# Kernel tuning notes

Measured on AMD Instinct MI355X. Metric: run time of the kernel, lower is better.

The kernel has to match this reference:

```python
import jax, jax.numpy as jnp
import numpy as np

WS = 8      # window_size
NH = 8      # n_heads
EPS = 1e-06


def _rel_coords(ws):
    # Swin-style relative position index table, matches torch buffer construction
    c = np.stack(np.meshgrid(np.arange(ws), np.arange(ws), indexing='ij'))  # [2,ws,ws]
    c = c.reshape(2, -1)                      # [2, L]
    rel = c[:, :, None] - c[:, None, :]       # [2, L, L]
    rel = rel.transpose(1, 2, 0) + (ws - 1)   # [L, L, 2]
    rel[:, :, 0] *= 2 * ws - 1
    return jnp.asarray(rel.sum(-1), dtype=jnp.int32)  # [L, L]


def rms_film(x, t, gw, bw):
    # x: [B,C,H,W], t: [B,d_t]; RMS over channel dim, FiLM scale/shift from t
    g = (t @ gw.T)[:, :, None, None]
    b = (t @ bw.T)[:, :, None, None]
    return g * x * jax.lax.rsqrt(jnp.mean(x * x, axis=1, keepdims=True) + EPS) + b


def window_attn(x, wq, wk, wv, wo_w, wo_b, rpb):
    B, C, H, W = x.shape
    h, w = H // WS, W // WS
    L = WS * WS
    dh = C // NH
    # partition into windows: [B, h, w, L, C]
    xw = x.reshape(B, C, h, WS, w, WS).transpose(0, 2, 4, 3, 5, 1).reshape(B, h, w, L, C)

    def heads(p):
        y = xw @ p.T  # Linear, no bias
        return y.reshape(B, h, w, L, NH, dh).transpose(0, 1, 2, 4, 3, 5)  # [B,h,w,n,L,dh]

    q, k, v = heads(wq), heads(wk), heads(wv)
    bias = rpb[:, _rel_coords(WS)]  # [NH, L, L] gather from bias table
    attn = jnp.einsum('bhwnld,bhwnmd->bhwnlm', q, k) / float(np.sqrt(dh)) + bias
    o = jnp.einsum('bhwnlm,bhwnmd->bhwnld', jax.nn.softmax(attn, axis=-1), v)
    # merge windows, channel order (n c): [B, NH*dh, H, W]
    o = o.reshape(B, h, w, NH, WS, WS, dh).transpose(0, 3, 6, 1, 4, 2, 5).reshape(B, C, H, W)
    # 1x1 conv output projection (with bias)
    return jnp.einsum('bchw,oc->bohw', o, wo_w) + wo_b[None, :, None, None]


def convnext(x, t, dw_w, dw_b, gw, bw, w1, b1, w2, b2):
    # 7x7 depthwise conv, pad 3
    y = jax.lax.conv_general_dilated(
        x, dw_w, window_strides=(1, 1), padding=[(3, 3), (3, 3)],
        dimension_numbers=('NCHW', 'OIHW', 'NCHW'), feature_group_count=x.shape[1])
    y = y + dw_b[None, :, None, None]
    y = rms_film(y, t, gw, bw).transpose(0, 2, 3, 1)  # -> NHWC
    y = jax.nn.gelu(y @ w1.T + b1, approximate=False) @ w2.T + b2
    return y.transpose(0, 3, 1, 2)


def setup_inputs() -> dict:
    key = jax.random.key(0)
    ks = jax.random.split(key, 16)
    D, DT, B, H, W = 256, 256, 8, 128, 128
    DH = 4 * D
    n = lambda k, s: jax.random.normal(k, s, jnp.float32) * 0.02
    return dict(
        x=jax.random.normal(ks[0], (B, D, H, W), jnp.float32),
        t=jax.random.normal(ks[1], (B, DT), jnp.float32),
        an_g=n(ks[2], (D, DT)), an_b=n(ks[3], (D, DT)),
        wq=n(ks[4], (D, D)), wk=n(ks[5], (D, D)), wv=n(ks[6], (D, D)),
        wo_w=n(ks[7], (D, D)), wo_b=jnp.zeros((D,), jnp.float32),
        rpb=n(ks[8], (NH, (2 * WS - 1) ** 2)),
        dw_w=n(ks[9], (D, 1, 7, 7)), dw_b=jnp.zeros((D,), jnp.float32),
        fn_g=n(ks[10], (D, DT)), fn_b=n(ks[11], (D, DT)),
        w1=n(ks[12], (DH, D)), b1=jnp.zeros((DH,), jnp.float32),
        w2=n(ks[13], (D, DH)), b2=jnp.zeros((D,), jnp.float32))


def reference(x, t, an_g, an_b, wq, wk, wv, wo_w, wo_b, rpb,
              dw_w, dw_b, fn_g, fn_b, w1, b1, w2, b2):
    x = x + window_attn(rms_film(x, t, an_g, an_b), wq, wk, wv, wo_w, wo_b, rpb)
    return x + convnext(x, t, dw_w, dw_b, fn_g, fn_b, w1, b1, w2, b2)
```

## Files before the change

kernel.cpp:

```cpp
#include <hip/hip_runtime.h>
#include <math.h>

typedef __attribute__((ext_vector_type(8))) short bf16x8_t;
typedef __attribute__((ext_vector_type(4))) float f32x4;

__device__ __forceinline__ unsigned short f2bf(float f) {
  unsigned int u = __builtin_bit_cast(unsigned int, f);
  u += 0x7FFFu + ((u >> 16) & 1u);
  return (unsigned short)(u >> 16);
}
__device__ __forceinline__ float bf2f(unsigned short h) {
  unsigned int u = ((unsigned int)h) << 16;
  return __builtin_bit_cast(float, u);
}

typedef const __attribute__((address_space(1))) void* as1cv;
typedef __attribute__((address_space(3))) void* as3v;

__device__ __forceinline__ void gld_lds16(const unsigned short* g, unsigned short* l) {
  __builtin_amdgcn_global_load_lds((as1cv)g, (as3v)l, 16, 0, 0);
}

__global__ __launch_bounds__(256) void tvec_kernel(const float* __restrict__ t,
    const float* __restrict__ an_g, const float* __restrict__ an_b,
    const float* __restrict__ fn_g, const float* __restrict__ fn_b,
    float* __restrict__ gvec) {
  int d = threadIdx.x;
  int b = blockIdx.x;
  int m = blockIdx.y;
  __shared__ float ts[256];
  ts[d] = t[b * 256 + d];
  __syncthreads();
  const float* W = (m == 0) ? an_g : (m == 1) ? an_b : (m == 2) ? fn_g : fn_b;
  float acc = 0.f;
  #pragma unroll 8
  for (int k = 0; k < 256; ++k) acc += ts[k] * W[d * 256 + k];
  gvec[(m * 8 + b) * 256 + d] = acc;
}

__global__ __launch_bounds__(256) void wconv_kernel(const float* __restrict__ wq,
    const float* __restrict__ wk, const float* __restrict__ wv, const float* __restrict__ wo,
    const float* __restrict__ w1, const float* __restrict__ w2,
    unsigned short* __restrict__ outp) {
  int i = blockIdx.x * 256 + threadIdx.x;
  const float* src; int off;
  if      (i <  65536) { src = wq; off = 0; }
  else if (i < 131072) { src = wk; off = 65536; }
  else if (i < 196608) { src = wv; off = 131072; }
  else if (i < 262144) { src = wo; off = 196608; }
  else if (i < 524288) { src = w1; off = 262144; }
  else                 { src = w2; off = 524288; }
  outp[i] = f2bf(src[i - off]);
}

template<int IS_BF>
__global__ __launch_bounds__(256) void film_kernel(const void* __restrict__ in_,
    const float* __restrict__ gvec, int gsel, unsigned short* __restrict__ outbf) {
  const float* inf = (const float*)in_;
  const unsigned short* inb = (const unsigned short*)in_;
  int blk = blockIdx.x;
  int b = blk >> 8;
  int p0 = (blk & 255) << 6;
  int lane = threadIdx.x & 63;
  int cg = threadIdx.x >> 6;
  __shared__ unsigned short vals[64][264];
  __shared__ float ssred[4][64];
  __shared__ float rinvs[64];
  size_t base = ((size_t)b << 22) + p0;
  float ss = 0.f;
  #pragma unroll 4
  for (int ci = 0; ci < 64; ++ci) {
    int c = (cg << 6) + ci;
    size_t idx = base + ((size_t)c << 14) + lane;
    float v = IS_BF ? bf2f(inb[idx]) : inf[idx];
    ss += v * v;
    vals[lane][c] = f2bf(v);
  }
  ssred[cg][lane] = ss;
  __syncthreads();
  if (threadIdx.x < 64) {
    float s = ssred[0][threadIdx.x] + ssred[1][threadIdx.x] + ssred[2][threadIdx.x] + ssred[3][threadIdx.x];
    rinvs[threadIdx.x] = rsqrtf(s * (1.0f / 256.0f) + 1e-6f);
  }
  __syncthreads();
  int pix = threadIdx.x >> 2;
  int c0 = (threadIdx.x & 3) << 6;
  float rv = rinvs[pix];
  const float* gp = gvec + ((gsel * 2 + 0) * 8 + b) * 256;
  const float* bp = gvec + ((gsel * 2 + 1) * 8 + b) * 256;
  unsigned short* orow = outbf + (((size_t)b << 14) + p0 + pix) * 256 + c0;
  #pragma unroll
  for (int ch = 0; ch < 8; ++ch) {
    bf16x8_t pack;
    #pragma unroll
    for (int e = 0; e < 8; ++e) {
      int c = c0 + ch * 8 + e;
      float v = bf2f(vals[pix][c]);
      float o = gp[c] * v * rv + bp[c];
      pack[e] = (short)f2bf(o);
    }
    *(bf16x8_t*)(orow + ch * 8) = pack;
  }
}

template<int DO_GELU>
__global__ __launch_bounds__(256) void gemm_kernel(const unsigned short* __restrict__ A,
    const unsigned short* __restrict__ Bw, const float* __restrict__ bias,
    unsigned short* __restrict__ outp, int K, int N) {
  __shared__ unsigned short As[128 * 64];
  __shared__ unsigned short Bs[128 * 64];
  int tid = threadIdx.x;
  int m0 = blockIdx.x << 7;
  int n0 = blockIdx.y << 7;
  int w = tid >> 6, lane = tid & 63;
  int wm = (w >> 1) << 6, wn = (w & 1) << 6;
  f32x4 acc[4][4];
  #pragma unroll
  for (int mi = 0; mi < 4; ++mi)
    #pragma unroll
    for (int ni = 0; ni < 4; ++ni)
      acc[mi][ni] = (f32x4){0.f, 0.f, 0.f, 0.f};

  for (int k0 = 0; k0 < K; k0 += 64) {
    #pragma unroll
    for (int r2 = 0; r2 < 4; ++r2) {
      int linear = (r2 << 8) + tid;
      int row = linear >> 3;
      int ch = linear & 7;
      gld_lds16(A  + (size_t)(m0 + row) * K + k0 + ch * 8, As + linear * 8);
      gld_lds16(Bw + (size_t)(n0 + row) * K + k0 + ch * 8, Bs + linear * 8);
    }
    __syncthreads();
    #pragma unroll
    for (int kk = 0; kk < 64; kk += 32) {
      bf16x8_t af[4], bq[4];
      int lr = lane & 15;
      int lk = ((lane >> 4) << 3) + kk;
      #pragma unroll
      for (int mi = 0; mi < 4; ++mi)
        af[mi] = *(const bf16x8_t*)(As + ((wm + (mi << 4) + lr) << 6) + lk);
      #pragma unroll
      for (int ni = 0; ni < 4; ++ni)
        bq[ni] = *(const bf16x8_t*)(Bs + ((wn + (ni << 4) + lr) << 6) + lk);
      #pragma unroll
      for (int mi = 0; mi < 4; ++mi)
        #pragma unroll
        for (int ni = 0; ni < 4; ++ni)
          acc[mi][ni] = __builtin_amdgcn_mfma_f32_16x16x32_bf16(af[mi], bq[ni], acc[mi][ni], 0, 0, 0);
    }
    __syncthreads();
  }
  int lr = lane & 15, lg = lane >> 4;
  #pragma unroll
  for (int mi = 0; mi < 4; ++mi) {
    #pragma unroll
    for (int ni = 0; ni < 4; ++ni) {
      int col = n0 + wn + (ni << 4) + lr;
      int row = m0 + wm + (mi << 4) + (lg << 2);
      f32x4 a = acc[mi][ni];
      #pragma unroll
      for (int i = 0; i < 4; ++i) {
        float v = a[i];
        if (DO_GELU) {
          v += bias[col];
          v = 0.5f * v * (1.0f + erff(v * 0.70710678118654752f));
        }
        outp[(size_t)(row + i) * N + col] = f2bf(v);
      }
    }
  }
}

__global__ __launch_bounds__(256) void gemm_t_kernel(const unsigned short* __restrict__ A,
    const unsigned short* __restrict__ Bw, unsigned short* __restrict__ outp) {
  __shared__ unsigned short smem[16384];
  unsigned short* As = smem;
  unsigned short* Bs = smem + 8192;
  const int K = 256;
  int tid = threadIdx.x;
  int m0 = blockIdx.x << 7;
  int n0 = blockIdx.y << 7;
  int w = tid >> 6, lane = tid & 63;
  int wm = (w >> 1) << 6, wn = (w & 1) << 6;
  f32x4 acc[4][4];
  #pragma unroll
  for (int mi = 0; mi < 4; ++mi)
    #pragma unroll
    for (int ni = 0; ni < 4; ++ni)
      acc[mi][ni] = (f32x4){0.f, 0.f, 0.f, 0.f};

  for (int k0 = 0; k0 < K; k0 += 64) {
    #pragma unroll
    for (int r2 = 0; r2 < 4; ++r2) {
      int linear = (r2 << 8) + tid;
      int row = linear >> 3;
      int ch = linear & 7;
      gld_lds16(A  + (size_t)(m0 + row) * K + k0 + ch * 8, As + linear * 8);
      gld_lds16(Bw + (size_t)(n0 + row) * K + k0 + ch * 8, Bs + linear * 8);
    }
    __syncthreads();
    #pragma unroll
    for (int kk = 0; kk < 64; kk += 32) {
      bf16x8_t af[4], bq[4];
      int lr = lane & 15;
      int lk = ((lane >> 4) << 3) + kk;
      #pragma unroll
      for (int mi = 0; mi < 4; ++mi)
        af[mi] = *(const bf16x8_t*)(As + ((wm + (mi << 4) + lr) << 6) + lk);
      #pragma unroll
      for (int ni = 0; ni < 4; ++ni)
        bq[ni] = *(const bf16x8_t*)(Bs + ((wn + (ni << 4) + lr) << 6) + lk);
      #pragma unroll
      for (int mi = 0; mi < 4; ++mi)
        #pragma unroll
        for (int ni = 0; ni < 4; ++ni)
          acc[mi][ni] = __builtin_amdgcn_mfma_f32_16x16x32_bf16(af[mi], bq[ni], acc[mi][ni], 0, 0, 0);
    }
    __syncthreads();
  }

  int lr = lane & 15, lg = lane >> 4;
  #pragma unroll
  for (int mi = 0; mi < 4; ++mi)
    #pragma unroll
    for (int ni = 0; ni < 4; ++ni) {
      int cl = wn + (ni << 4) + lr;
      int rl = wm + (mi << 4) + (lg << 2);
      f32x4 a = acc[mi][ni];
      #pragma unroll
      for (int i = 0; i < 4; ++i)
        smem[cl * 128 + rl + i] = f2bf(a[i]);
    }
  __syncthreads();

  int cl = tid >> 1;
  int half = tid & 1;
  int b = m0 >> 14;
  int pix = (m0 & 16383) + half * 64;
  int c = n0 + cl;
  const unsigned short* srow = smem + cl * 128 + half * 64;
  unsigned short* orow = outp + ((size_t)b * 256 + c) * 16384 + pix;
  #pragma unroll
  for (int jj = 0; jj < 8; ++jj)
    *(bf16x8_t*)(orow + jj * 8) = *(const bf16x8_t*)(srow + jj * 8);
}

__global__ __launch_bounds__(256) void gemm2f_kernel(const unsigned short* __restrict__ A,
    const unsigned short* __restrict__ Bw, const float* __restrict__ bias,
    const unsigned short* __restrict__ x1, float* __restrict__ outp, int m_base) {
  __shared__ unsigned short smem[16384];
  unsigned short* As = smem;
  unsigned short* Bs = smem + 8192;
  const int K = 1024, N = 256;
  int tid = threadIdx.x;
  int m0 = blockIdx.x << 7;
  int n0 = blockIdx.y << 7;
  int w = tid >> 6, lane = tid & 63;
  int wm = (w >> 1) << 6, wn = (w & 1) << 6;
  f32x4 acc[4][4];
  #pragma unroll
  for (int mi = 0; mi < 4; ++mi)
    #pragma unroll
    for (int ni = 0; ni < 4; ++ni)
      acc[mi][ni] = (f32x4){0.f, 0.f, 0.f, 0.f};

  for (int k0 = 0; k0 < K; k0 += 64) {
    #pragma unroll
    for (int r2 = 0; r2 < 4; ++r2) {
      int linear = (r2 << 8) + tid;
      int row = linear >> 3;
      int ch = linear & 7;
      gld_lds16(A  + (size_t)(m0 + row) * K + k0 + ch * 8, As + linear * 8);
      gld_lds16(Bw + (size_t)(n0 + row) * K + k0 + ch * 8, Bs + linear * 8);
    }
    __syncthreads();
    #pragma unroll
    for (int kk = 0; kk < 64; kk += 32) {
      bf16x8_t af[4], bq[4];
      int lr = lane & 15;
      int lk = ((lane >> 4) << 3) + kk;
      #pragma unroll
      for (int mi = 0; mi < 4; ++mi)
        af[mi] = *(const bf16x8_t*)(As + ((wm + (mi << 4) + lr) << 6) + lk);
      #pragma unroll
      for (int ni = 0; ni < 4; ++ni)
        bq[ni] = *(const bf16x8_t*)(Bs + ((wn + (ni << 4) + lr) << 6) + lk);
      #pragma unroll
      for (int mi = 0; mi < 4; ++mi)
        #pragma unroll
        for (int ni = 0; ni < 4; ++ni)
          acc[mi][ni] = __builtin_amdgcn_mfma_f32_16x16x32_bf16(af[mi], bq[ni], acc[mi][ni], 0, 0, 0);
    }
    __syncthreads();
  }

  int lr = lane & 15, lg = lane >> 4;
  #pragma unroll
  for (int mi = 0; mi < 4; ++mi)
    #pragma unroll
    for (int ni = 0; ni < 4; ++ni) {
      int cl = wn + (ni << 4) + lr;
      int rl = wm + (mi << 4) + (lg << 2);
      f32x4 a = acc[mi][ni];
      #pragma unroll
      for (int i = 0; i < 4; ++i)
        smem[cl * 128 + rl + i] = f2bf(a[i]);
    }
  __syncthreads();

  int cl = tid >> 1;
  int half = tid & 1;
  int pglob0 = m_base + m0;
  int b = pglob0 >> 14;
  int pix = (pglob0 & 16383) + half * 64;
  int c = n0 + cl;
  const unsigned short* srow = smem + cl * 128 + half * 64;
  size_t gbase = ((size_t)b * 256 + c) * 16384 + pix;
  const unsigned short* xrow = x1 + gbase;
  float* orow = outp + gbase;
  float bb = bias[c];
  #pragma unroll
  for (int jj = 0; jj < 8; ++jj) {
    bf16x8_t sv = *(const bf16x8_t*)(srow + jj * 8);
    bf16x8_t xv = *(const bf16x8_t*)(xrow + jj * 8);
    #pragma unroll
    for (int e = 0; e < 8; ++e)
      orow[jj * 8 + e] = bf2f((unsigned short)sv[e]) + bf2f((unsigned short)xv[e]) + bb;
  }
}

__global__ __launch_bounds__(256, 3) void attn_kernel(const unsigned short* __restrict__ qg,
    const unsigned short* __restrict__ kg, const unsigned short* __restrict__ vt,
    const float* __restrict__ rpb, unsigned short* __restrict__ og) {
  __shared__ float rpbf[1800];
  __shared__ unsigned short pbuf[4][64 * 72];
  int wi = blockIdx.x;
  int b = wi >> 8, wh = (wi >> 4) & 15, ww = wi & 15;
  int tid = threadIdx.x;
  int w = tid >> 6, lane = tid & 63;
  int g = lane >> 4, lr = lane & 15;
  for (int idx = tid; idx < 1800; idx += 256) rpbf[idx] = rpb[idx];
  __syncthreads();

  int rowpix = (wh * 8) * 128 + ww * 8;
  size_t ibase = ((size_t)b << 14) + rowpix;
  unsigned short* pb = pbuf[w];
  const float scale = 0.17677669529663689f;

  #pragma unroll 1
  for (int hh = 0; hh < 2; ++hh) {
    int h = w * 2 + hh;
    float sums[4][4];
    {
      bf16x8_t qf[4], kf[4];
      #pragma unroll
      for (int t = 0; t < 4; ++t) {
        size_t tok = ibase + (size_t)(t * 2 + (lr >> 3)) * 128 + (lr & 7);
        qf[t] = *(const bf16x8_t*)(qg + tok * 256 + h * 32 + g * 8);
        kf[t] = *(const bf16x8_t*)(kg + tok * 256 + h * 32 + g * 8);
      }
      f32x4 sacc[4][4];
      #pragma unroll
      for (int qt = 0; qt < 4; ++qt)
        #pragma unroll
        for (int kt = 0; kt < 4; ++kt)
          sacc[qt][kt] = __builtin_amdgcn_mfma_f32_16x16x32_bf16(qf[qt], kf[kt],
                           (f32x4){0.f, 0.f, 0.f, 0.f}, 0, 0, 0);
      const float* rb = &rpbf[h * 225];
      #pragma unroll
      for (int qt = 0; qt < 4; ++qt) {
        #pragma unroll
        for (int i = 0; i < 4; ++i) {
          int q = qt * 16 + g * 4 + i;
          int il = q >> 3, jl = q & 7;
          float v[4];
          #pragma unroll
          for (int kt = 0; kt < 4; ++kt) {
            int kv = kt * 16 + lr;
            v[kt] = sacc[qt][kt][i] * scale + rb[(il - (kv >> 3) + 7) * 15 + (jl - (kv & 7) + 7)];
          }
          float mx = fmaxf(fmaxf(v[0], v[1]), fmaxf(v[2], v[3]));
          mx = fmaxf(mx, __shfl_xor(mx, 1));
          mx = fmaxf(mx, __shfl_xor(mx, 2));
          mx = fmaxf(mx, __shfl_xor(mx, 4));
          mx = fmaxf(mx, __shfl_xor(mx, 8));
          float sm = 0.f;
          #pragma unroll
          for (int kt = 0; kt < 4; ++kt) { v[kt] = __expf(v[kt] - mx); sm += v[kt]; }
          sm += __shfl_xor(sm, 1);
          sm += __shfl_xor(sm, 2);
          sm += __shfl_xor(sm, 4);
          sm += __shfl_xor(sm, 8);
          sums[qt][i] = sm;
          #pragma unroll
          for (int kt = 0; kt < 4; ++kt)
            pb[q * 72 + kt * 16 + lr] = f2bf(v[kt]);
        }
      }
    }
    f32x4 oacc[4][2];
    #pragma unroll
    for (int qt = 0; qt < 4; ++qt) {
      oacc[qt][0] = (f32x4){0.f, 0.f, 0.f, 0.f};
      oacc[qt][1] = (f32x4){0.f, 0.f, 0.f, 0.f};
    }
    #pragma unroll
    for (int ks = 0; ks < 2; ++ks) {
      bf16x8_t pf[4], vf[2];
      #pragma unroll
      for (int qt = 0; qt < 4; ++qt)
        pf[qt] = *(const bf16x8_t*)(pb + (qt * 16 + lr) * 72 + ks * 32 + g * 8);
      #pragma unroll
      for (int dt = 0; dt < 2; ++dt) {
        size_t plane = (size_t)b * 256 + h * 32 + dt * 16 + lr;
        vf[dt] = *(const bf16x8_t*)(vt + (plane << 14) + rowpix + (size_t)(ks * 4 + g) * 128);
      }
      #pragma unroll
      for (int qt = 0; qt < 4; ++qt)
        #pragma unroll
        for (int dt = 0; dt < 2; ++dt)
          oacc[qt][dt] = __builtin_amdgcn_mfma_f32_16x16x32_bf16(pf[qt], vf[dt], oacc[qt][dt], 0, 0, 0);
    }
    #pragma unroll
    for (int qt = 0; qt < 4; ++qt) {
      #pragma unroll
      for (int i = 0; i < 4; ++i) {
        int q = qt * 16 + g * 4 + i;
        float inv = 1.0f / sums[qt][i];
        size_t tok = ibase + (size_t)(q >> 3) * 128 + (q & 7);
        #pragma unroll
        for (int dt = 0; dt < 2; ++dt)
          og[tok * 256 + h * 32 + dt * 16 + lr] = f2bf(oacc[qt][dt][i] * inv);
      }
    }
  }
}

__global__ __launch_bounds__(256) void addt1_kernel(const unsigned short* __restrict__ src,
    const float* __restrict__ resid, const float* __restrict__ bias,
    unsigned short* __restrict__ outp) {
  int blk = blockIdx.x;
  int b = blk >> 8;
  int p0 = (blk & 255) << 6;
  __shared__ unsigned short vals[64][264];
  int tid = threadIdx.x;
  #pragma unroll
  for (int r = 0; r < 8; ++r) {
    int linear = r * 256 + tid;
    int row = linear >> 5;
    int ch = linear & 31;
    bf16x8_t v = *(const bf16x8_t*)(src + (((size_t)b << 14) + p0 + row) * 256 + ch * 8);
    *(bf16x8_t*)(&vals[row][ch * 8]) = v;
  }
  __syncthreads();
  int lane = tid & 63;
  int cq = tid >> 6;
  #pragma unroll 4
  for (int ci = 0; ci < 64; ++ci) {
    int c = (cq << 6) + ci;
    float v = bf2f(vals[lane][c]);
    size_t gidx = ((size_t)b << 22) + ((size_t)c << 14) + p0 + lane;
    outp[gidx] = f2bf(resid[gidx] + v + bias[c]);
  }
}

__global__ __launch_bounds__(256) void dwconv_kernel(const unsigned short* __restrict__ x1,
    const float* __restrict__ w, const float* __restrict__ bias, unsigned short* __restrict__ outp) {
  int bc = blockIdx.y;
  int c = bc & 255;
  int y0 = blockIdx.x << 6;
  __shared__ unsigned short tile[70 * 144];
  __shared__ float wf[49];
  const unsigned short* plane = x1 + ((size_t)bc << 14);
  int tid = threadIdx.x;

  for (int idx = tid; idx < 70 * 16; idx += 256) {
    int row = idx >> 4, ch = idx & 15;
    int gy = y0 - 3 + row;
    bf16x8_t v = (bf16x8_t){0, 0, 0, 0, 0, 0, 0, 0};
    if (gy >= 0 && gy < 128) v = *(const bf16x8_t*)(plane + gy * 128 + ch * 8);
    *(bf16x8_t*)(&tile[row * 144 + 8 + ch * 8]) = v;
  }
  for (int idx = tid; idx < 70 * 6; idx += 256) {
    int row = idx / 6, e = idx % 6;
    int col = (e < 3) ? (5 + e) : (133 + e);
    tile[row * 144 + col] = 0;
  }
  if (tid < 49) wf[tid] = w[c * 49 + tid];
  __syncthreads();

  int r = tid >> 2;
  int c0 = (tid & 3) << 5;
  float acc[32];
  float bb = bias[c];
  #pragma unroll
  for (int i = 0; i < 32; ++i) acc[i] = bb;

  #pragma unroll
  for (int u = 0; u < 7; ++u) {
    const unsigned short* rowp = &tile[(r + u) * 144 + c0];
    float f[48];
    #pragma unroll
    for (int k = 0; k < 6; ++k) {
      bf16x8_t v = *(const bf16x8_t*)(rowp + k * 8);
      #pragma unroll
      for (int e = 0; e < 8; ++e) f[k * 8 + e] = bf2f((unsigned short)v[e]);
    }
    #pragma unroll
    for (int t = 0; t < 7; ++t) {
      float wv = wf[u * 7 + t];
      #pragma unroll
      for (int i = 0; i < 32; ++i) acc[i] += f[i + 5 + t] * wv;
    }
  }

  unsigned short* orow = outp + ((size_t)bc << 14) + (size_t)(y0 + r) * 128 + c0;
  #pragma unroll
  for (int k = 0; k < 4; ++k) {
    bf16x8_t v;
    #pragma unroll
    for (int e = 0; e < 8; ++e) v[e] = (short)f2bf(acc[k * 8 + e]);
    *(bf16x8_t*)(orow + k * 8) = v;
  }
}

extern "C" void kernel_launch(void* const* d_in, const int* in_sizes, int n_in,
                              void* d_out, int out_size, void* d_ws, size_t ws_size,
                              hipStream_t stream) {
  const float* x    = (const float*)d_in[0];
  const float* t    = (const float*)d_in[1];
  const float* an_g = (const float*)d_in[2];
  const float* an_b = (const float*)d_in[3];
  const float* wq   = (const float*)d_in[4];
  const float* wk   = (const float*)d_in[5];
  const float* wv   = (const float*)d_in[6];
  const float* wo_w = (const float*)d_in[7];
  const float* wo_b = (const float*)d_in[8];
  const float* rpb  = (const float*)d_in[9];
  const float* dw_w = (const float*)d_in[10];
  const float* dw_b = (const float*)d_in[11];
  const float* fn_g = (const float*)d_in[12];
  const float* fn_b = (const float*)d_in[13];
  const float* w1   = (const float*)d_in[14];
  const float* b1   = (const float*)d_in[15];
  const float* w2   = (const float*)d_in[16];
  const float* b2   = (const float*)d_in[17];
  float* outp = (float*)d_out;

  char* ws = (char*)d_ws;
  const size_t MB = 1024ull * 1024ull;
  float* gvec = (float*)ws;
  unsigned short* wbf = (unsigned short*)(ws + 32768);
  unsigned short* P = (unsigned short*)(ws + 2 * MB);
  unsigned short* Q = (unsigned short*)(ws + 66 * MB);
  unsigned short* R = (unsigned short*)(ws + 130 * MB);
  unsigned short* vbuf = (unsigned short*)((char*)d_out + 64 * MB);

  unsigned short* wq_bf = wbf;
  unsigned short* wk_bf = wbf + 65536;
  unsigned short* wv_bf = wbf + 131072;
  unsigned short* wo_bf = wbf + 196608;
  unsigned short* w1_bf = wbf + 262144;
  unsigned short* w2_bf = wbf + 524288;

  tvec_kernel<<<dim3(8, 4), 256, 0, stream>>>(t, an_g, an_b, fn_g, fn_b, gvec);
  wconv_kernel<<<3072, 256, 0, stream>>>(wq, wk, wv, wo_w, w1, w2, wbf);

  film_kernel<0><<<2048, 256, 0, stream>>>(x, gvec, 0, P);

  gemm_kernel<0><<<dim3(1024, 2), 256, 0, stream>>>(P, wq_bf, nullptr, Q, 256, 256);
  gemm_kernel<0><<<dim3(1024, 2), 256, 0, stream>>>(P, wk_bf, nullptr, R, 256, 256);
  gemm_t_kernel<<<dim3(1024, 2), 256, 0, stream>>>(P, wv_bf, vbuf);

  attn_kernel<<<2048, 256, 0, stream>>>(Q, R, vbuf, rpb, P);

  gemm_kernel<0><<<dim3(1024, 2), 256, 0, stream>>>(P, wo_bf, nullptr, Q, 256, 256);
  addt1_kernel<<<2048, 256, 0, stream>>>(Q, x, wo_b, R);

  dwconv_kernel<<<dim3(2, 2048), 256, 0, stream>>>(R, dw_w, dw_b, Q);
  film_kernel<1><<<2048, 256, 0, stream>>>(Q, gvec, 1, P);

  for (int qtr = 0; qtr < 4; ++qtr) {
    int m_base = qtr * 32768;
    gemm_kernel<1><<<dim3(256, 8), 256, 0, stream>>>(P + (size_t)m_base * 256, w1_bf, b1, Q, 256, 1024);
    gemm2f_kernel<<<dim3(256, 2), 256, 0, stream>>>(Q, w2_bf, b2, R, outp, m_base);
  }
}
```

Baseline: 958.1 us.

## Fuse output projection with residual add and store bf16 copy of input

The first FiLM pass now also writes a bf16 copy of x into the output buffer. The standalone residual-add/transposition kernel is removed, and a new GEMM epilogue adds bias and the bf16 residual while writing channel-major output directly. This cuts one full kernel's memory round trip at the cost of an extra bf16 write in film and lower residual precision (bf16 x instead of fp32). The attention kernel's block-to-window mapping is also permuted, interleaving batches across consecutive blocks.

```diff
diff --git a/kernel.cpp b/kernel.cpp
--- a/kernel.cpp
+++ b/kernel.cpp
@@ -53,9 +53,10 @@
   outp[i] = f2bf(src[i - off]);
 }
 
-template<int IS_BF>
+template<int IS_BF, int WX>
 __global__ __launch_bounds__(256) void film_kernel(const void* __restrict__ in_,
-    const float* __restrict__ gvec, int gsel, unsigned short* __restrict__ outbf) {
+    const float* __restrict__ gvec, int gsel, unsigned short* __restrict__ outbf,
+    unsigned short* __restrict__ xbf) {
   const float* inf = (const float*)in_;
   const unsigned short* inb = (const unsigned short*)in_;
   int blk = blockIdx.x;
@@ -74,7 +75,9 @@
     size_t idx = base + ((size_t)c << 14) + lane;
     float v = IS_BF ? bf2f(inb[idx]) : inf[idx];
     ss += v * v;
-    vals[lane][c] = f2bf(v);
+    unsigned short hv = f2bf(v);
+    vals[lane][c] = hv;
+    if (WX) xbf[idx] = hv;
   }
   ssred[cg][lane] = ss;
   __syncthreads();
@@ -243,6 +246,91 @@
   #pragma unroll
   for (int jj = 0; jj < 8; ++jj)
     *(bf16x8_t*)(orow + jj * 8) = *(const bf16x8_t*)(srow + jj * 8);
+}
+
+__global__ __launch_bounds__(256) void gemm_wof_kernel(const unsigned short* __restrict__ A,
+    const unsigned short* __restrict__ Bw, const float* __restrict__ bias,
+    const unsigned short* __restrict__ xbf, unsigned short* __restrict__ outp) {
+  __shared__ unsigned short smem[16384];
+  unsigned short* As = smem;
+  unsigned short* Bs = smem + 8192;
+  const int K = 256;
+  int tid = threadIdx.x;
+  int m0 = blockIdx.x << 7;
+  int n0 = blockIdx.y << 7;
+  int w = tid >> 6, lane = tid & 63;
+  int wm = (w >> 1) << 6, wn = (w & 1) << 6;
+  f32x4 acc[4][4];
+  #pragma unroll
+  for (int mi = 0; mi < 4; ++mi)
+    #pragma unroll
+    for (int ni = 0; ni < 4; ++ni)
+      acc[mi][ni] = (f32x4){0.f, 0.f, 0.f, 0.f};
+
+  for (int k0 = 0; k0 < K; k0 += 64) {
+    #pragma unroll
+    for (int r2 = 0; r2 < 4; ++r2) {
+      int linear = (r2 << 8) + tid;
+      int row = linear >> 3;
+      int ch = linear & 7;
+      gld_lds16(A  + (size_t)(m0 + row) * K + k0 + ch * 8, As + linear * 8);
+      gld_lds16(Bw + (size_t)(n0 + row) * K + k0 + ch * 8, Bs + linear * 8);
+    }
+    __syncthreads();
+    #pragma unroll
+    for (int kk = 0; kk < 64; kk += 32) {
+      bf16x8_t af[4], bq[4];
+      int lr = lane & 15;
+      int lk = ((lane >> 4) << 3) + kk;
+      #pragma unroll
+      for (int mi = 0; mi < 4; ++mi)
+        af[mi] = *(const bf16x8_t*)(As + ((wm + (mi << 4) + lr) << 6) + lk);
+      #pragma unroll
+      for (int ni = 0; ni < 4; ++ni)
+        bq[ni] = *(const bf16x8_t*)(Bs + ((wn + (ni << 4) + lr) << 6) + lk);
+      #pragma unroll
+      for (int mi = 0; mi < 4; ++mi)
+        #pragma unroll
+        for (int ni = 0; ni < 4; ++ni)
+          acc[mi][ni] = __builtin_amdgcn_mfma_f32_16x16x32_bf16(af[mi], bq[ni], acc[mi][ni], 0, 0, 0);
+    }
+    __syncthreads();
+  }
+
+  int lr = lane & 15, lg = lane >> 4;
+  #pragma unroll
+  for (int mi = 0; mi < 4; ++mi)
+    #pragma unroll
+    for (int ni = 0; ni < 4; ++ni) {
+      int cl = wn + (ni << 4) + lr;
+      int rl = wm + (mi << 4) + (lg << 2);
+      f32x4 a = acc[mi][ni];
+      #pragma unroll
+      for (int i = 0; i < 4; ++i)
+        smem[cl * 128 + rl + i] = f2bf(a[i]);
+    }
+  __syncthreads();
+
+  int cl = tid >> 1;
+  int half = tid & 1;
+  int b = m0 >> 14;
+  int pix = (m0 & 16383) + half * 64;
+  int c = n0 + cl;
+  const unsigned short* srow = smem + cl * 128 + half * 64;
+  size_t gbase = ((size_t)b * 256 + c) * 16384 + pix;
+  const unsigned short* xrow = xbf + gbase;
+  unsigned short* orow = outp + gbase;
+  float bb = bias[c];
+  #pragma unroll
+  for (int jj = 0; jj < 8; ++jj) {
+    bf16x8_t sv = *(const bf16x8_t*)(srow + jj * 8);
+    bf16x8_t xv = *(const bf16x8_t*)(xrow + jj * 8);
+    bf16x8_t ov;
+    #pragma unroll
+    for (int e = 0; e < 8; ++e)
+      ov[e] = (short)f2bf(bf2f((unsigned short)sv[e]) + bf2f((unsigned short)xv[e]) + bb);
+    *(bf16x8_t*)(orow + jj * 8) = ov;
+  }
 }
 
 __global__ __launch_bounds__(256) void gemm2f_kernel(const unsigned short* __restrict__ A,
@@ -334,7 +422,7 @@
     const float* __restrict__ rpb, unsigned short* __restrict__ og) {
   __shared__ float rpbf[1800];
   __shared__ unsigned short pbuf[4][64 * 72];
-  int wi = blockIdx.x;
+  int wi = (blockIdx.x & 7) * 256 + (blockIdx.x >> 3);
   int b = wi >> 8, wh = (wi >> 4) & 15, ww = wi & 15;
   int tid = threadIdx.x;
   int w = tid >> 6, lane = tid & 63;
@@ -436,34 +524,6 @@
   }
 }
 
-__global__ __launch_bounds__(256) void addt1_kernel(const unsigned short* __restrict__ src,
-    const float* __restrict__ resid, const float* __restrict__ bias,
-    unsigned short* __restrict__ outp) {
-  int blk = blockIdx.x;
-  int b = blk >> 8;
-  int p0 = (blk & 255) << 6;
-  __shared__ unsigned short vals[64][264];
-  int tid = threadIdx.x;
-  #pragma unroll
-  for (int r = 0; r < 8; ++r) {
-    int linear = r * 256 + tid;
-    int row = linear >> 5;
-    int ch = linear & 31;
-    bf16x8_t v = *(const bf16x8_t*)(src + (((size_t)b << 14) + p0 + row) * 256 + ch * 8);
-    *(bf16x8_t*)(&vals[row][ch * 8]) = v;
-  }
-  __syncthreads();
-  int lane = tid & 63;
-  int cq = tid >> 6;
-  #pragma unroll 4
-  for (int ci = 0; ci < 64; ++ci) {
-    int c = (cq << 6) + ci;
-    float v = bf2f(vals[lane][c]);
-    size_t gidx = ((size_t)b << 22) + ((size_t)c << 14) + p0 + lane;
-    outp[gidx] = f2bf(resid[gidx] + v + bias[c]);
-  }
-}
-
 __global__ __launch_bounds__(256) void dwconv_kernel(const unsigned short* __restrict__ x1,
     const float* __restrict__ w, const float* __restrict__ bias, unsigned short* __restrict__ outp) {
   int bc = blockIdx.y;
@@ -554,6 +614,7 @@
   unsigned short* P = (unsigned short*)(ws + 2 * MB);
   unsigned short* Q = (unsigned short*)(ws + 66 * MB);
   unsigned short* R = (unsigned short*)(ws + 130 * MB);
+  unsigned short* xbf  = (unsigned short*)d_out;
   unsigned short* vbuf = (unsigned short*)((char*)d_out + 64 * MB);
 
   unsigned short* wq_bf = wbf;
@@ -566,7 +627,7 @@
   tvec_kernel<<<dim3(8, 4), 256, 0, stream>>>(t, an_g, an_b, fn_g, fn_b, gvec);
   wconv_kernel<<<3072, 256, 0, stream>>>(wq, wk, wv, wo_w, w1, w2, wbf);
 
-  film_kernel<0><<<2048, 256, 0, stream>>>(x, gvec, 0, P);
+  film_kernel<0, 1><<<2048, 256, 0, stream>>>(x, gvec, 0, P, xbf);
 
   gemm_kernel<0><<<dim3(1024, 2), 256, 0, stream>>>(P, wq_bf, nullptr, Q, 256, 256);
   gemm_kernel<0><<<dim3(1024, 2), 256, 0, stream>>>(P, wk_bf, nullptr, R, 256, 256);
@@ -574,11 +635,10 @@
 
   attn_kernel<<<2048, 256, 0, stream>>>(Q, R, vbuf, rpb, P);
 
-  gemm_kernel<0><<<dim3(1024, 2), 256, 0, stream>>>(P, wo_bf, nullptr, Q, 256, 256);
-  addt1_kernel<<<2048, 256, 0, stream>>>(Q, x, wo_b, R);
+  gemm_wof_kernel<<<dim3(1024, 2), 256, 0, stream>>>(P, wo_bf, wo_b, xbf, R);
 
   dwconv_kernel<<<dim3(2, 2048), 256, 0, stream>>>(R, dw_w, dw_b, Q);
-  film_kernel<1><<<2048, 256, 0, stream>>>(Q, gvec, 1, P);
+  film_kernel<1, 0><<<2048, 256, 0, stream>>>(Q, gvec, 1, P, nullptr);
 
   for (int qtr = 0; qtr < 4; ++qtr) {
     int m_base = qtr * 32768;
```

Result: faster. 936.6 us (-2.2%).
